# Kernel tuning notes

Measured on AMD Instinct MI355X. Metric: run time of the kernel, lower is better.

Reference implementation:

```python
import jax, jax.numpy as jnp
import numpy as np

NEG = -1e6  # masked_softmax fill value from the torch source


def setup_inputs() -> dict:
    key = jax.random.key(0)
    ks = jax.random.split(key, 7)
    B, NQ, NK, D, H = 4, 256, 1024, 256, 256
    queries = jax.random.normal(ks[0], (B, NQ, D), dtype=jnp.float32)
    keys_ = jax.random.normal(ks[1], (B, NK, D), dtype=jnp.float32)
    values = jax.random.normal(ks[2], (B, NK, D), dtype=jnp.float32)
    valid_lens = jax.random.randint(ks[3], (B,), 1, NK + 1, dtype=jnp.int32)
    scale = 1.0 / np.sqrt(D)
    Wq = jax.random.normal(ks[4], (D, H), dtype=jnp.float32) * scale
    Wk = jax.random.normal(ks[5], (D, H), dtype=jnp.float32) * scale
    w_v = jax.random.normal(ks[6], (H,), dtype=jnp.float32) * (1.0 / np.sqrt(H))
    return {"queries": queries, "keys": keys_, "values": values,
            "valid_lens": valid_lens, "Wq": Wq, "Wk": Wk, "w_v": w_v}


def reference(queries, keys, values, valid_lens, Wq, Wk, w_v):
    # projections
    q = jnp.einsum('bqd,dh->bqh', queries, Wq)           # [B,NQ,H]
    k = jnp.einsum('bkd,dh->bkh', keys, Wk)              # [B,NK,H]
    # broadcast-add + tanh + dense(->1): scores [B,NQ,NK]
    features = jnp.tanh(q[:, :, None, :] + k[:, None, :, :])  # [B,NQ,NK,H]
    scores = jnp.einsum('bqkh,h->bqk', features, w_v)
    # masked softmax over last axis with per-batch valid lengths
    nk = keys.shape[1]
    mask = jnp.arange(nk)[None, None, :] < valid_lens[:, None, None]  # [B,1,NK]
    scores = jnp.where(mask, scores, NEG)
    attn = jax.nn.softmax(scores, axis=-1)               # [B,NQ,NK]
    # dropout in eval mode -> identity
    return jnp.einsum('bqk,bkd->bqd', attn, values)      # [B,NQ,D]
```

## Files before the change

### kernel.cpp

```cpp
#include <hip/hip_runtime.h>
#include <hip/hip_fp16.h>
#include <math.h>

#define BB 4
#define NQ 256
#define NK 1024
#define DD 256
#define HH 256

#define TMR 32
#define TNC 64
#define TKK 16
#define NT (DD / TKK)

__global__ __launch_bounds__(256) void proj_exp_kernel(
    const float* __restrict__ Q, const float* __restrict__ K,
    const float* __restrict__ Wq, const float* __restrict__ Wk,
    const int* __restrict__ vlen,
    __half* __restrict__ Eq, __half* __restrict__ Ek)
{
    const int QROWT = (BB * NQ) / TMR;
    int bx = blockIdx.x;
    int rt = bx >> 2, ct = bx & 3;
    const float* A; const float* W; __half* C; int bm;
    if (rt < QROWT) { A = Q; W = Wq; C = Eq; bm = rt * TMR; }
    else {
        int kt = rt - QROWT;
        int b = kt >> 5;
        int lr = (kt & 31) * TMR;
        if (lr >= vlen[b]) return;
        A = K; W = Wk; C = Ek; bm = kt * TMR;
    }
    int bn = ct * TNC;

    __shared__ float As[2][TKK][TMR + 2];
    __shared__ float Ws[2][TKK][TNC + 4];

    int tid = threadIdx.x;
    int ar = (tid >> 2) & 31, ac4 = tid & 3;
    int wkk = tid >> 4, wc4 = tid & 15;
    int ty = tid >> 4, tx = tid & 15;

    float4 aR = {0,0,0,0}, wR;
    if (tid < 128) aR = *(const float4*)&A[(size_t)(bm + ar) * DD + ac4 * 4];
    wR = *(const float4*)&W[(size_t)wkk * HH + bn + wc4 * 4];

    float acc[2][4] = {};

    for (int t = 0; t < NT; ++t) {
        int cur = t & 1;
        if (tid < 128) {
            As[cur][ac4 * 4 + 0][ar] = aR.x;
            As[cur][ac4 * 4 + 1][ar] = aR.y;
            As[cur][ac4 * 4 + 2][ar] = aR.z;
            As[cur][ac4 * 4 + 3][ar] = aR.w;
        }
        *(float4*)&Ws[cur][wkk][wc4 * 4] = wR;
        if (t + 1 < NT) {
            int k0 = (t + 1) * TKK;
            if (tid < 128)
                aR = *(const float4*)&A[(size_t)(bm + ar) * DD + k0 + ac4 * 4];
            wR = *(const float4*)&W[(size_t)(k0 + wkk) * HH + bn + wc4 * 4];
        }
        __syncthreads();
#pragma unroll
        for (int kk = 0; kk < TKK; ++kk) {
            float2 a2 = *(const float2*)&As[cur][kk][ty * 2];
            float4 w4 = *(const float4*)&Ws[cur][kk][tx * 4];
            acc[0][0] = fmaf(a2.x, w4.x, acc[0][0]);
            acc[0][1] = fmaf(a2.x, w4.y, acc[0][1]);
            acc[0][2] = fmaf(a2.x, w4.z, acc[0][2]);
            acc[0][3] = fmaf(a2.x, w4.w, acc[0][3]);
            acc[1][0] = fmaf(a2.y, w4.x, acc[1][0]);
            acc[1][1] = fmaf(a2.y, w4.y, acc[1][1]);
            acc[1][2] = fmaf(a2.y, w4.z, acc[1][2]);
            acc[1][3] = fmaf(a2.y, w4.w, acc[1][3]);
        }
    }

#pragma unroll
    for (int i = 0; i < 2; ++i) {
        int m = bm + ty * 2 + i;
        __half h[4];
#pragma unroll
        for (int j = 0; j < 4; ++j)
            h[j] = __float2half(__expf(2.f * fminf(fmaxf(acc[i][j], -5.5f), 5.5f)));
        *(ushort4*)&C[(size_t)m * HH + bn + tx * 4] = *(ushort4*)h;
    }
}

__global__ __launch_bounds__(256) void scores_kernel(
    const __half* __restrict__ Eq, const __half* __restrict__ Ek,
    const float* __restrict__ wv, const int* __restrict__ vlen,
    float* __restrict__ P, float* __restrict__ Psum)
{
    __shared__ __align__(16) __half sQ[32][HH + 8];
    __shared__ __align__(16) __half sK[32][HH + 8];
    __shared__ __align__(16) float sW[HH];

    int bid = blockIdx.x;
    int b = bid & 3;
    int rest = bid >> 2;
    int qc = rest & 7;
    int kc = rest >> 3;
    int L = vlen[b];
    int k0 = kc * 32;
    if (k0 >= L) return;
    int q0 = qc * 32;

    int tid = threadIdx.x;
    {
        int c8 = tid & 31;
        int r0 = tid >> 5;
        const __half* gq = Eq + ((size_t)b * NQ + q0) * HH;
        const __half* gk = Ek + ((size_t)b * NK + k0) * HH;
#pragma unroll
        for (int i = 0; i < 4; ++i) {
            int r = r0 + 8 * i;
            *(uint4*)&sQ[r][c8 * 8] = *(const uint4*)&gq[(size_t)r * HH + c8 * 8];
            *(uint4*)&sK[r][c8 * 8] = *(const uint4*)&gk[(size_t)r * HH + c8 * 8];
        }
        sW[tid] = wv[tid];
    }
    __syncthreads();

    int ki = tid & 15, qi = tid >> 4;
    float a00 = 0.f, a01 = 0.f, a10 = 0.f, a11 = 0.f;

#pragma unroll 4
    for (int h4 = 0; h4 < HH / 4; ++h4) {
        float4 w = *(const float4*)&sW[h4 * 4];
        float wxy = w.x + w.y, wzw = w.z + w.w;
        float2 q0a = __half22float2(*(const __half2*)&sQ[qi][h4 * 4]);
        float2 q0b = __half22float2(*(const __half2*)&sQ[qi][h4 * 4 + 2]);
        float2 q1a = __half22float2(*(const __half2*)&sQ[qi + 16][h4 * 4]);
        float2 q1b = __half22float2(*(const __half2*)&sQ[qi + 16][h4 * 4 + 2]);
        float2 k0a = __half22float2(*(const __half2*)&sK[ki][h4 * 4]);
        float2 k0b = __half22float2(*(const __half2*)&sK[ki][h4 * 4 + 2]);
        float2 k1a = __half22float2(*(const __half2*)&sK[ki + 16][h4 * 4]);
        float2 k1b = __half22float2(*(const __half2*)&sK[ki + 16][h4 * 4 + 2]);
        float4 A0 = {q0a.x, q0a.y, q0b.x, q0b.y};
        float4 A1 = {q1a.x, q1a.y, q1b.x, q1b.y};
        float4 B0 = {k0a.x, k0a.y, k0b.x, k0b.y};
        float4 B1 = {k1a.x, k1a.y, k1b.x, k1b.y};
#define QUAD(acc, Aq, Bk)                                                    \
        {                                                                    \
            float E1 = Aq.x * Bk.x, E2 = Aq.y * Bk.y;                        \
            float E3 = Aq.z * Bk.z, E4 = Aq.w * Bk.w;                        \
            float d1 = E1 + 1.f, d2 = E2 + 1.f;                              \
            float d3 = E3 + 1.f, d4 = E4 + 1.f;                              \
            float n12 = fmaf(w.x, E2, fmaf(w.y, E1, wxy));                   \
            float n34 = fmaf(w.z, E4, fmaf(w.w, E3, wzw));                   \
            float d12 = d1 * d2, d34 = d3 * d4;                              \
            float num = fmaf(n12, d34, n34 * d12);                           \
            acc = fmaf(num, __builtin_amdgcn_rcpf(d12 * d34), acc);          \
        }
        QUAD(a00, A0, B0);
        QUAD(a01, A0, B1);
        QUAD(a10, A1, B0);
        QUAD(a11, A1, B1);
#undef QUAD
    }

    int kA = k0 + ki, kB = kA + 16;
    float p00 = (kA < L) ? __expf(-2.f * a00) : 0.f;
    float p10 = (kA < L) ? __expf(-2.f * a10) : 0.f;
    float p01 = (kB < L) ? __expf(-2.f * a01) : 0.f;
    float p11 = (kB < L) ? __expf(-2.f * a11) : 0.f;

    float* s0 = P + ((size_t)b * NQ + q0 + qi) * NK;
    float* s1 = P + ((size_t)b * NQ + q0 + qi + 16) * NK;
    s0[kA] = p00; s0[kB] = p01;
    s1[kA] = p10; s1[kB] = p11;

    float r0s = p00 + p01, r1s = p10 + p11;
#pragma unroll
    for (int o = 1; o <= 8; o <<= 1) {
        r0s += __shfl_xor(r0s, o, 64);
        r1s += __shfl_xor(r1s, o, 64);
    }
    if (ki == 0) {
        Psum[((size_t)b * NQ + q0 + qi) * 32 + kc] = r0s;
        Psum[((size_t)b * NQ + q0 + qi + 16) * 32 + kc] = r1s;
    }
}

__global__ __launch_bounds__(256) void pv_kernel(
    const float* __restrict__ P, const float* __restrict__ V,
    const float* __restrict__ Psum, const int* __restrict__ vlen,
    float* __restrict__ out)
{
    __shared__ __align__(16) float sPt[2][32][36];
    __shared__ __align__(16) float sV[2][32][36];
    __shared__ float sAll[3][64][17];
    __shared__ float sRowsum[32];

    int bid = blockIdx.x;
    int b = bid & 3;
    int rest = bid >> 2;
    int qt = rest >> 3, dt = rest & 7;
    int q0 = qt * 32, d0 = dt * 32;
    int L = vlen[b];
    int nc = (L + 31) >> 5;

    int tid = threadIdx.x;
    if (tid < 32) {
        float s = 0.f;
        const float* pp = Psum + ((size_t)b * NQ + q0 + tid) * 32;
        for (int c = 0; c < nc; ++c) s += pp[c];
        sRowsum[tid] = s;
    }

    int r = tid >> 3, c4 = tid & 7;
    int w = tid >> 6, sp = tid & 63;
    int qg = sp >> 3, dg = sp & 7;

    const float* Pb = P + ((size_t)b * NQ + q0 + r) * NK;
    const float* Vb = V + (size_t)b * NK * DD + d0;

    float4 pf = *(const float4*)(Pb + c4 * 4);
    float4 vf = *(const float4*)(Vb + (size_t)r * DD + c4 * 4);

    float acc[4][4] = {};

    for (int c = 0; c < nc; ++c) {
        int cur = c & 1;
        sPt[cur][c4 * 4 + 0][r] = pf.x;
        sPt[cur][c4 * 4 + 1][r] = pf.y;
        sPt[cur][c4 * 4 + 2][r] = pf.z;
        sPt[cur][c4 * 4 + 3][r] = pf.w;
        *(float4*)&sV[cur][r][c4 * 4] = vf;
        if (c + 1 < nc) {
            int kn = (c + 1) * 32;
            pf = *(const float4*)(Pb + kn + c4 * 4);
            vf = *(const float4*)(Vb + (size_t)(kn + r) * DD + c4 * 4);
        }
        __syncthreads();
#pragma unroll
        for (int kk = 0; kk < 8; ++kk) {
            float4 A  = *(const float4*)&sPt[cur][w * 8 + kk][qg * 4];
            float4 Bv = *(const float4*)&sV[cur][w * 8 + kk][dg * 4];
            acc[0][0] = fmaf(A.x, Bv.x, acc[0][0]);
            acc[0][1] = fmaf(A.x, Bv.y, acc[0][1]);
            acc[0][2] = fmaf(A.x, Bv.z, acc[0][2]);
            acc[0][3] = fmaf(A.x, Bv.w, acc[0][3]);
            acc[1][0] = fmaf(A.y, Bv.x, acc[1][0]);
            acc[1][1] = fmaf(A.y, Bv.y, acc[1][1]);
            acc[1][2] = fmaf(A.y, Bv.z, acc[1][2]);
            acc[1][3] = fmaf(A.y, Bv.w, acc[1][3]);
            acc[2][0] = fmaf(A.z, Bv.x, acc[2][0]);
            acc[2][1] = fmaf(A.z, Bv.y, acc[2][1]);
            acc[2][2] = fmaf(A.z, Bv.z, acc[2][2]);
            acc[2][3] = fmaf(A.z, Bv.w, acc[2][3]);
            acc[3][0] = fmaf(A.w, Bv.x, acc[3][0]);
            acc[3][1] = fmaf(A.w, Bv.y, acc[3][1]);
            acc[3][2] = fmaf(A.w, Bv.z, acc[3][2]);
            acc[3][3] = fmaf(A.w, Bv.w, acc[3][3]);
        }
    }

    if (w > 0) {
#pragma unroll
        for (int i = 0; i < 4; ++i)
#pragma unroll
            for (int j = 0; j < 4; ++j) sAll[w - 1][sp][i * 4 + j] = acc[i][j];
    }
    __syncthreads();
    if (w == 0) {
#pragma unroll
        for (int ww = 0; ww < 3; ++ww)
#pragma unroll
            for (int i = 0; i < 4; ++i)
#pragma unroll
                for (int j = 0; j < 4; ++j) acc[i][j] += sAll[ww][sp][i * 4 + j];
#pragma unroll
        for (int i = 0; i < 4; ++i) {
            float inv = 1.0f / sRowsum[qg * 4 + i];
            float4 o = { acc[i][0] * inv, acc[i][1] * inv,
                         acc[i][2] * inv, acc[i][3] * inv };
            *(float4*)&out[((size_t)b * NQ + q0 + qg * 4 + i) * DD + d0 + dg * 4] = o;
        }
    }
}

extern "C" void kernel_launch(void* const* d_in, const int* in_sizes, int n_in,
                              void* d_out, int out_size, void* d_ws, size_t ws_size,
                              hipStream_t stream) {
    const float* queries = (const float*)d_in[0];
    const float* keys    = (const float*)d_in[1];
    const float* values  = (const float*)d_in[2];
    const int*   vlens   = (const int*)d_in[3];
    const float* Wq      = (const float*)d_in[4];
    const float* Wk      = (const float*)d_in[5];
    const float* wv      = (const float*)d_in[6];
    float* out = (float*)d_out;

    __half* Eqh = (__half*)d_ws;
    __half* Ekh = Eqh + (size_t)BB * NQ * HH;
    float*  P    = (float*)(Ekh + (size_t)BB * NK * HH);
    float*  Psum = P + (size_t)BB * NQ * NK;

    proj_exp_kernel<<<dim3(((BB * NQ) / TMR + (BB * NK) / TMR) * 4), 256, 0,
                      stream>>>(queries, keys, Wq, Wk, vlens, Eqh, Ekh);

    scores_kernel<<<dim3(BB * (NQ / 32) * (NK / 32)), 256, 0, stream>>>(
        Eqh, Ekh, wv, vlens, P, Psum);

    pv_kernel<<<dim3(BB * (NQ / 32) * (DD / 32)), 256, 0, stream>>>(
        P, values, Psum, vlens, out);
}
```

Baseline: 57.21 us.

## Rewrite projection GEMM using fp16 MFMA with transposed weight tile in LDS

```diff
diff --git a/kernel.cpp b/kernel.cpp
--- a/kernel.cpp
+++ b/kernel.cpp
@@ -8,84 +8,103 @@
 #define DD 256
 #define HH 256
 
-#define TMR 32
-#define TNC 64
-#define TKK 16
-#define NT (DD / TKK)
-
-__global__ __launch_bounds__(256) void proj_exp_kernel(
+typedef __attribute__((ext_vector_type(8))) _Float16 f16x8;
+typedef __attribute__((ext_vector_type(4))) _Float16 f16x4;
+typedef __attribute__((ext_vector_type(4))) float f32x4;
+
+__global__ __launch_bounds__(256) void proj_mfma_kernel(
     const float* __restrict__ Q, const float* __restrict__ K,
     const float* __restrict__ Wq, const float* __restrict__ Wk,
     const int* __restrict__ vlen,
     __half* __restrict__ Eq, __half* __restrict__ Ek)
 {
-    const int QROWT = (BB * NQ) / TMR;
     int bx = blockIdx.x;
-    int rt = bx >> 2, ct = bx & 3;
-    const float* A; const float* W; __half* C; int bm;
-    if (rt < QROWT) { A = Q; W = Wq; C = Eq; bm = rt * TMR; }
+    int mt = bx >> 3, nt = bx & 7;
+    const float *A, *W; __half* C; int bm;
+    if (mt < 16) { A = Q; W = Wq; C = Eq; bm = mt * 64; }
     else {
-        int kt = rt - QROWT;
-        int b = kt >> 5;
-        int lr = (kt & 31) * TMR;
+        int kt = mt - 16;
+        int b = kt >> 4;
+        int lr = (kt & 15) * 64;
         if (lr >= vlen[b]) return;
-        A = K; W = Wk; C = Ek; bm = kt * TMR;
-    }
-    int bn = ct * TNC;
-
-    __shared__ float As[2][TKK][TMR + 2];
-    __shared__ float Ws[2][TKK][TNC + 4];
+        A = K; W = Wk; C = Ek; bm = kt * 64;
+    }
+    int bn = nt * 32;
+
+    __shared__ __half Wt[32][260];
 
     int tid = threadIdx.x;
-    int ar = (tid >> 2) & 31, ac4 = tid & 3;
-    int wkk = tid >> 4, wc4 = tid & 15;
-    int ty = tid >> 4, tx = tid & 15;
-
-    float4 aR = {0,0,0,0}, wR;
-    if (tid < 128) aR = *(const float4*)&A[(size_t)(bm + ar) * DD + ac4 * 4];
-    wR = *(const float4*)&W[(size_t)wkk * HH + bn + wc4 * 4];
-
-    float acc[2][4] = {};
-
-    for (int t = 0; t < NT; ++t) {
-        int cur = t & 1;
-        if (tid < 128) {
-            As[cur][ac4 * 4 + 0][ar] = aR.x;
-            As[cur][ac4 * 4 + 1][ar] = aR.y;
-            As[cur][ac4 * 4 + 2][ar] = aR.z;
-            As[cur][ac4 * 4 + 3][ar] = aR.w;
-        }
-        *(float4*)&Ws[cur][wkk][wc4 * 4] = wR;
-        if (t + 1 < NT) {
-            int k0 = (t + 1) * TKK;
-            if (tid < 128)
-                aR = *(const float4*)&A[(size_t)(bm + ar) * DD + k0 + ac4 * 4];
-            wR = *(const float4*)&W[(size_t)(k0 + wkk) * HH + bn + wc4 * 4];
-        }
-        __syncthreads();
-#pragma unroll
-        for (int kk = 0; kk < TKK; ++kk) {
-            float2 a2 = *(const float2*)&As[cur][kk][ty * 2];
-            float4 w4 = *(const float4*)&Ws[cur][kk][tx * 4];
-            acc[0][0] = fmaf(a2.x, w4.x, acc[0][0]);
-            acc[0][1] = fmaf(a2.x, w4.y, acc[0][1]);
-            acc[0][2] = fmaf(a2.x, w4.z, acc[0][2]);
-            acc[0][3] = fmaf(a2.x, w4.w, acc[0][3]);
-            acc[1][0] = fmaf(a2.y, w4.x, acc[1][0]);
-            acc[1][1] = fmaf(a2.y, w4.y, acc[1][1]);
-            acc[1][2] = fmaf(a2.y, w4.z, acc[1][2]);
-            acc[1][3] = fmaf(a2.y, w4.w, acc[1][3]);
-        }
-    }
-
-#pragma unroll
-    for (int i = 0; i < 2; ++i) {
-        int m = bm + ty * 2 + i;
-        __half h[4];
-#pragma unroll
-        for (int j = 0; j < 4; ++j)
-            h[j] = __float2half(__expf(2.f * fminf(fmaxf(acc[i][j], -5.5f), 5.5f)));
-        *(ushort4*)&C[(size_t)m * HH + bn + tx * 4] = *(ushort4*)h;
+    {
+        int dp = tid >> 3, cg = tid & 7;
+#pragma unroll
+        for (int pp = 0; pp < 4; ++pp) {
+            int d0r = (dp + pp * 32) * 2;
+            float4 r0 = *(const float4*)&W[(size_t)d0r * HH + bn + cg * 4];
+            float4 r1 = *(const float4*)&W[(size_t)(d0r + 1) * HH + bn + cg * 4];
+            int n = cg * 4;
+            *(__half2*)&Wt[n + 0][d0r] = __floats2half2_rn(r0.x, r1.x);
+            *(__half2*)&Wt[n + 1][d0r] = __floats2half2_rn(r0.y, r1.y);
+            *(__half2*)&Wt[n + 2][d0r] = __floats2half2_rn(r0.z, r1.z);
+            *(__half2*)&Wt[n + 3][d0r] = __floats2half2_rn(r0.w, r1.w);
+        }
+    }
+    __syncthreads();
+
+    int lane = tid & 63, w = tid >> 6;
+    int wm = w & 1, wn = w >> 1;
+    int lm = lane & 15, lk = (lane >> 4) * 4;
+
+    const float* arow0 = A + (size_t)(bm + wm * 32 + lm) * DD;
+    const float* arow1 = arow0 + (size_t)16 * DD;
+    const __half* brow = &Wt[wn * 16 + lm][0];
+
+    f32x4 acc0 = {0.f, 0.f, 0.f, 0.f};
+    f32x4 acc1 = {0.f, 0.f, 0.f, 0.f};
+
+    float4 a00 = *(const float4*)(arow0 + lk);
+    float4 a01 = *(const float4*)(arow0 + 16 + lk);
+    float4 a10 = *(const float4*)(arow1 + lk);
+    float4 a11 = *(const float4*)(arow1 + 16 + lk);
+    f16x4 b0 = *(const f16x4*)&brow[lk];
+    f16x4 b1 = *(const f16x4*)&brow[16 + lk];
+
+#pragma unroll
+    for (int s = 0; s < 8; ++s) {
+        float4 c00 = a00, c01 = a01, c10 = a10, c11 = a11;
+        f16x4 cb0 = b0, cb1 = b1;
+        if (s < 7) {
+            int d = (s + 1) * 32;
+            a00 = *(const float4*)(arow0 + d + lk);
+            a01 = *(const float4*)(arow0 + d + 16 + lk);
+            a10 = *(const float4*)(arow1 + d + lk);
+            a11 = *(const float4*)(arow1 + d + 16 + lk);
+            b0 = *(const f16x4*)&brow[d + lk];
+            b1 = *(const f16x4*)&brow[d + 16 + lk];
+        }
+        f16x8 af0, af1, bf;
+        af0[0] = (_Float16)c00.x; af0[1] = (_Float16)c00.y;
+        af0[2] = (_Float16)c00.z; af0[3] = (_Float16)c00.w;
+        af0[4] = (_Float16)c01.x; af0[5] = (_Float16)c01.y;
+        af0[6] = (_Float16)c01.z; af0[7] = (_Float16)c01.w;
+        af1[0] = (_Float16)c10.x; af1[1] = (_Float16)c10.y;
+        af1[2] = (_Float16)c10.z; af1[3] = (_Float16)c10.w;
+        af1[4] = (_Float16)c11.x; af1[5] = (_Float16)c11.y;
+        af1[6] = (_Float16)c11.z; af1[7] = (_Float16)c11.w;
+        bf[0] = cb0[0]; bf[1] = cb0[1]; bf[2] = cb0[2]; bf[3] = cb0[3];
+        bf[4] = cb1[0]; bf[5] = cb1[1]; bf[6] = cb1[2]; bf[7] = cb1[3];
+        acc0 = __builtin_amdgcn_mfma_f32_16x16x32_f16(af0, bf, acc0, 0, 0, 0);
+        acc1 = __builtin_amdgcn_mfma_f32_16x16x32_f16(af1, bf, acc1, 0, 0, 0);
+    }
+
+    int mB0 = bm + wm * 32 + (lane >> 4) * 4;
+    int mB1 = mB0 + 16;
+    int n = bn + wn * 16 + lm;
+#pragma unroll
+    for (int r = 0; r < 4; ++r) {
+        float e0 = __expf(2.f * fminf(fmaxf(acc0[r], -5.5f), 5.5f));
+        float e1 = __expf(2.f * fminf(fmaxf(acc1[r], -5.5f), 5.5f));
+        C[(size_t)(mB0 + r) * HH + n] = __float2half(e0);
+        C[(size_t)(mB1 + r) * HH + n] = __float2half(e1);
     }
 }
 
@@ -300,8 +319,8 @@
     float*  P    = (float*)(Ekh + (size_t)BB * NK * HH);
     float*  Psum = P + (size_t)BB * NQ * NK;
 
-    proj_exp_kernel<<<dim3(((BB * NQ) / TMR + (BB * NK) / TMR) * 4), 256, 0,
-                      stream>>>(queries, keys, Wq, Wk, vlens, Eqh, Ekh);
+    proj_mfma_kernel<<<dim3(640), 256, 0, stream>>>(
+        queries, keys, Wq, Wk, vlens, Eqh, Ekh);
 
     scores_kernel<<<dim3(BB * (NQ / 32) * (NK / 32)), 256, 0, stream>>>(
         Eqh, Ekh, wv, vlens, P, Psum);
```

New measurement: 54.93 us. 1.04x faster.
